# Kernel tuning notes

Hardware: AMD Instinct MI355X
Metric: run time of the kernel (lower is better)

Reference implementation:

```python
import jax, jax.numpy as jnp
import numpy as np


def setup_inputs() -> dict:
    key = jax.random.key(0)
    k1, k2 = jax.random.split(key)
    B, H, W = 4, 512, 512
    win = 5
    x = jax.random.normal(k1, (B, 3, H, W), dtype=jnp.float32)
    f = jax.random.uniform(k2, (B, win * win, H, W), dtype=jnp.float32)
    return {"x": x, "f": f, "window": win}


def reference(x, f, window):
    # x: [B, 3, H, W], f: [B, window^2, H, W]
    w = window
    p = w // 2
    B, C, H, W = x.shape
    xp = jnp.pad(x, ((0, 0), (0, 0), (p, p), (p, p)))  # ZeroPad2d(w//2)
    # One-hot conv2d == extract the (i, j) shifted window for each of w*w taps.
    # patches: [B, C, w*w, H, W]; tap order matches build_window (row-major).
    patches = jnp.stack(
        [xp[:, :, i:i + H, j:j + W] for i in range(w) for j in range(w)],
        axis=2,
    )
    # Per-pixel weighted sum over the w*w taps, same filter f for each color.
    y = jnp.einsum('bckhw,bkhw->bchw', patches, f)
    return y
```

## Files before the change

kernel.cpp:

```cpp
#include <hip/hip_runtime.h>

#define Bd   4
#define Cc   3
#define Hd   512
#define Wd   512
#define WIN  5
#define PAD  2
#define PLANE (Hd * Wd)

#define TW   128
#define TH   8
#define LDS_COLS (TW + 2 * PAD)
#define LDS_ROWS (TH + 2 * PAD)

typedef float f4 __attribute__((ext_vector_type(4)));

__global__ __launch_bounds__(256, 4) void filter_layer_kernel(
    const float* __restrict__ x,
    const float* __restrict__ f,
    float* __restrict__ y)
{
    __shared__ __align__(16) float xs[Cc][LDS_ROWS][LDS_COLS];

    const int b  = blockIdx.z;
    const int h0 = blockIdx.y * TH;
    const int w0 = blockIdx.x * TW;
    const int tid = threadIdx.x;

    const int tile_n = Cc * LDS_ROWS * LDS_COLS;
    for (int idx = tid; idx < tile_n; idx += 256) {
        const int col = idx % LDS_COLS;
        const int t   = idx / LDS_COLS;
        const int row = t % LDS_ROWS;
        const int c   = t / LDS_ROWS;
        const int gh  = h0 + row - PAD;
        const int gw  = w0 + col - PAD;
        float v = 0.0f;
        if (gh >= 0 && gh < Hd && gw >= 0 && gw < Wd)
            v = x[(((size_t)b * Cc + c) * Hd + gh) * Wd + gw];
        xs[c][row][col] = v;
    }
    __syncthreads();

    const int tx   = tid & 31;
    const int ty   = tid >> 5;
    const int wloc = tx * 4;
    const int h    = h0 + ty;
    const int gw   = w0 + wloc;

    const float* fb = f + ((size_t)b * (WIN * WIN)) * PLANE
                        + (size_t)h * Wd + gw;

    float acc[Cc][4];
    #pragma unroll
    for (int c = 0; c < Cc; ++c)
        #pragma unroll
        for (int p = 0; p < 4; ++p) acc[c][p] = 0.0f;

    f4 fcur[WIN], fnxt[WIN];
    #pragma unroll
    for (int j = 0; j < WIN; ++j)
        fcur[j] = __builtin_nontemporal_load(
            (const f4*)(fb + (size_t)j * PLANE));

    #pragma unroll 1
    for (int i = 0; i < WIN; ++i) {
        if (i + 1 < WIN) {
            const float* fr = fb + (size_t)(i + 1) * WIN * PLANE;
            #pragma unroll
            for (int j = 0; j < WIN; ++j)
                fnxt[j] = __builtin_nontemporal_load(
                    (const f4*)(fr + (size_t)j * PLANE));
        }

        float xr[Cc][8];
        #pragma unroll
        for (int c = 0; c < Cc; ++c) {
            const f4* src = (const f4*)&xs[c][ty + i][wloc];
            const f4 a  = src[0];
            const f4 b4 = src[1];
            xr[c][0] = a.x;  xr[c][1] = a.y;  xr[c][2] = a.z;  xr[c][3] = a.w;
            xr[c][4] = b4.x; xr[c][5] = b4.y; xr[c][6] = b4.z; xr[c][7] = b4.w;
        }

        #pragma unroll
        for (int j = 0; j < WIN; ++j) {
            const f4 fv = fcur[j];
            #pragma unroll
            for (int c = 0; c < Cc; ++c) {
                acc[c][0] += fv.x * xr[c][j + 0];
                acc[c][1] += fv.y * xr[c][j + 1];
                acc[c][2] += fv.z * xr[c][j + 2];
                acc[c][3] += fv.w * xr[c][j + 3];
            }
        }

        #pragma unroll
        for (int j = 0; j < WIN; ++j) fcur[j] = fnxt[j];
    }

    #pragma unroll
    for (int c = 0; c < Cc; ++c) {
        f4 o;
        o.x = acc[c][0]; o.y = acc[c][1]; o.z = acc[c][2]; o.w = acc[c][3];
        *(f4*)(y + (((size_t)b * Cc + c) * Hd + h) * Wd + gw) = o;
    }
}

extern "C" void kernel_launch(void* const* d_in, const int* in_sizes, int n_in,
                              void* d_out, int out_size, void* d_ws, size_t ws_size,
                              hipStream_t stream) {
    const float* x = (const float*)d_in[0];
    const float* f = (const float*)d_in[1];
    float* y = (float*)d_out;

    dim3 grid(Wd / TW, Hd / TH, Bd);
    filter_layer_kernel<<<grid, dim3(256), 0, stream>>>(x, f, y);
}
```

Measured before the change: 167.0 us.

## Use full-width row tiles with 8 pixels per thread and vectorized halo load

Each block now covers four full 512-wide rows instead of a 128x8 tile, so the horizontal halo disappears and the LDS fill becomes coalesced float4 loads with only the edge pads zeroed. Each thread computes 8 pixels instead of 4, doubling the filter loads in flight and the register usage, with launch bounds lowered to 2 blocks per SIMD. Nontemporal loads of the filter are replaced with ordinary loads. The intent is to cut the scalar index math and halo overhead and raise memory-level parallelism on this streaming, bandwidth-bound kernel, at the cost of fewer blocks (512) and lower occupancy.

```diff
diff --git a/kernel.cpp b/kernel.cpp
--- a/kernel.cpp
+++ b/kernel.cpp
@@ -1,109 +1,116 @@
 #include <hip/hip_runtime.h>
 
-#define Bd   4
-#define Cc   3
-#define Hd   512
-#define Wd   512
-#define WIN  5
-#define PAD  2
+#define Bd    4
+#define Cc    3
+#define Hd    512
+#define Wd    512
+#define WIN   5
 #define PLANE (Hd * Wd)
 
-#define TW   128
-#define TH   8
-#define LDS_COLS (TW + 2 * PAD)
-#define LDS_ROWS (TH + 2 * PAD)
+#define TH    4
+#define LROWS (TH + 4)
+#define LROW  520
 
 typedef float f4 __attribute__((ext_vector_type(4)));
 
-__global__ __launch_bounds__(256, 4) void filter_layer_kernel(
+__global__ __launch_bounds__(256, 2) void filter_layer_kernel(
     const float* __restrict__ x,
     const float* __restrict__ f,
     float* __restrict__ y)
 {
-    __shared__ __align__(16) float xs[Cc][LDS_ROWS][LDS_COLS];
+    __shared__ __align__(16) float xs[Cc][LROWS][LROW];
 
-    const int b  = blockIdx.z;
-    const int h0 = blockIdx.y * TH;
-    const int w0 = blockIdx.x * TW;
+    const int b   = blockIdx.y;
+    const int h0  = blockIdx.x * TH;
     const int tid = threadIdx.x;
 
-    const int tile_n = Cc * LDS_ROWS * LDS_COLS;
-    for (int idx = tid; idx < tile_n; idx += 256) {
-        const int col = idx % LDS_COLS;
-        const int t   = idx / LDS_COLS;
-        const int row = t % LDS_ROWS;
-        const int c   = t / LDS_ROWS;
-        const int gh  = h0 + row - PAD;
-        const int gw  = w0 + col - PAD;
-        float v = 0.0f;
-        if (gh >= 0 && gh < Hd && gw >= 0 && gw < Wd)
-            v = x[(((size_t)b * Cc + c) * Hd + gh) * Wd + gw];
-        xs[c][row][col] = v;
+    {
+        const int lane32 = tid & 31;
+        const int rowi   = tid >> 5;
+        const int gh     = h0 + rowi - 2;
+        const bool hok   = (gh >= 0) && (gh < Hd);
+        #pragma unroll
+        for (int c = 0; c < Cc; ++c) {
+            const float* xrow = x + (((size_t)b * Cc + c) * Hd + gh) * Wd;
+            #pragma unroll
+            for (int g = 0; g < 4; ++g) {
+                const int gw = (g * 32 + lane32) * 4;
+                f4 v = {0.f, 0.f, 0.f, 0.f};
+                if (hok) v = *(const f4*)(xrow + gw);
+                *(f4*)&xs[c][rowi][gw + 4] = v;
+            }
+            if (lane32 == 0) {
+                xs[c][rowi][2]   = 0.f; xs[c][rowi][3]   = 0.f;
+                xs[c][rowi][516] = 0.f; xs[c][rowi][517] = 0.f;
+            }
+        }
     }
     __syncthreads();
 
-    const int tx   = tid & 31;
-    const int ty   = tid >> 5;
-    const int wloc = tx * 4;
-    const int h    = h0 + ty;
-    const int gw   = w0 + wloc;
+    const int lane = tid & 63;
+    const int rw   = tid >> 6;
+    const int h    = h0 + rw;
+    const int px0  = lane * 8;
 
-    const float* fb = f + ((size_t)b * (WIN * WIN)) * PLANE
-                        + (size_t)h * Wd + gw;
+    const float* fb = f + ((size_t)b * WIN * WIN) * PLANE
+                        + (size_t)h * Wd + px0;
 
-    float acc[Cc][4];
+    float acc[Cc][8];
     #pragma unroll
     for (int c = 0; c < Cc; ++c)
         #pragma unroll
-        for (int p = 0; p < 4; ++p) acc[c][p] = 0.0f;
+        for (int p = 0; p < 8; ++p) acc[c][p] = 0.f;
 
-    f4 fcur[WIN], fnxt[WIN];
+    f4 fc[2 * WIN], fn[2 * WIN];
     #pragma unroll
-    for (int j = 0; j < WIN; ++j)
-        fcur[j] = __builtin_nontemporal_load(
-            (const f4*)(fb + (size_t)j * PLANE));
+    for (int j = 0; j < WIN; ++j) {
+        fc[2 * j]     = *(const f4*)(fb + (size_t)j * PLANE);
+        fc[2 * j + 1] = *(const f4*)(fb + (size_t)j * PLANE + 4);
+    }
 
     #pragma unroll 1
     for (int i = 0; i < WIN; ++i) {
         if (i + 1 < WIN) {
             const float* fr = fb + (size_t)(i + 1) * WIN * PLANE;
             #pragma unroll
-            for (int j = 0; j < WIN; ++j)
-                fnxt[j] = __builtin_nontemporal_load(
-                    (const f4*)(fr + (size_t)j * PLANE));
+            for (int j = 0; j < WIN; ++j) {
+                fn[2 * j]     = *(const f4*)(fr + (size_t)j * PLANE);
+                fn[2 * j + 1] = *(const f4*)(fr + (size_t)j * PLANE + 4);
+            }
         }
 
-        float xr[Cc][8];
+        float xr[Cc][16];
         #pragma unroll
-        for (int c = 0; c < Cc; ++c) {
-            const f4* src = (const f4*)&xs[c][ty + i][wloc];
-            const f4 a  = src[0];
-            const f4 b4 = src[1];
-            xr[c][0] = a.x;  xr[c][1] = a.y;  xr[c][2] = a.z;  xr[c][3] = a.w;
-            xr[c][4] = b4.x; xr[c][5] = b4.y; xr[c][6] = b4.z; xr[c][7] = b4.w;
-        }
+        for (int c = 0; c < Cc; ++c)
+            #pragma unroll
+            for (int g = 0; g < 4; ++g)
+                *(f4*)&xr[c][g * 4] = *(const f4*)&xs[c][rw + i][px0 + g * 4];
 
         #pragma unroll
         for (int j = 0; j < WIN; ++j) {
-            const f4 fv = fcur[j];
             #pragma unroll
             for (int c = 0; c < Cc; ++c) {
-                acc[c][0] += fv.x * xr[c][j + 0];
-                acc[c][1] += fv.y * xr[c][j + 1];
-                acc[c][2] += fv.z * xr[c][j + 2];
-                acc[c][3] += fv.w * xr[c][j + 3];
+                #pragma unroll
+                for (int p = 0; p < 8; ++p) {
+                    const float fv = (p < 4)
+                        ? ((const float*)&fc[2 * j])[p]
+                        : ((const float*)&fc[2 * j + 1])[p - 4];
+                    acc[c][p] += fv * xr[c][p + j + 2];
+                }
             }
         }
 
         #pragma unroll
-        for (int j = 0; j < WIN; ++j) fcur[j] = fnxt[j];
+        for (int t = 0; t < 2 * WIN; ++t) fc[t] = fn[t];
     }
 
     #pragma unroll
     for (int c = 0; c < Cc; ++c) {
-        f4 o;
-        o.x = acc[c][0]; o.y = acc[c][1]; o.z = acc[c][2]; o.w = acc[c][3];
-        *(f4*)(y + (((size_t)b * Cc + c) * Hd + h) * Wd + gw) = o;
+        float* yp = y + (((size_t)b * Cc + c) * Hd + h) * Wd + px0;
+        f4 o0 = {acc[c][0], acc[c][1], acc[c][2], acc[c][3]};
+        f4 o1 = {acc[c][4], acc[c][5], acc[c][6], acc[c][7]};
+        *(f4*)yp       = o0;
+        *(f4*)(yp + 4) = o1;
     }
 }
 
@@ -114,6 +121,6 @@
     const float* f = (const float*)d_in[1];
     float* y = (float*)d_out;
 
-    dim3 grid(Wd / TW, Hd / TH, Bd);
+    dim3 grid(Hd / TH, Bd);
     filter_layer_kernel<<<grid, dim3(256), 0, stream>>>(x, f, y);
 }
```

Result: no change. 168.5 us (+0.9%).

## Drop LDS staging; read x halo directly from global per row

Applied to the files above, without the earlier changes.

Removes the shared-memory tile and barrier. Each 128-thread block now handles one full image row and loads neighbouring x vectors straight from global memory (L1/L2 cached), with boundary guards. Output is written with nontemporal stores. This trades the LDS fill and sync for redundant global x reads across rows and threads, relying on caches to absorb them, while the dominant f stream stays the same.

```diff
diff --git a/kernel.cpp b/kernel.cpp
--- a/kernel.cpp
+++ b/kernel.cpp
@@ -1,67 +1,35 @@
 #include <hip/hip_runtime.h>
 
-#define Bd   4
-#define Cc   3
-#define Hd   512
-#define Wd   512
-#define WIN  5
-#define PAD  2
+#define Bd    4
+#define Cc    3
+#define Hd    512
+#define Wd    512
+#define WIN   5
 #define PLANE (Hd * Wd)
-
-#define TW   128
-#define TH   8
-#define LDS_COLS (TW + 2 * PAD)
-#define LDS_ROWS (TH + 2 * PAD)
 
 typedef float f4 __attribute__((ext_vector_type(4)));
 
-__global__ __launch_bounds__(256, 4) void filter_layer_kernel(
+__global__ __launch_bounds__(128, 4) void filter_layer_kernel(
     const float* __restrict__ x,
     const float* __restrict__ f,
     float* __restrict__ y)
 {
-    __shared__ __align__(16) float xs[Cc][LDS_ROWS][LDS_COLS];
-
-    const int b  = blockIdx.z;
-    const int h0 = blockIdx.y * TH;
-    const int w0 = blockIdx.x * TW;
-    const int tid = threadIdx.x;
-
-    const int tile_n = Cc * LDS_ROWS * LDS_COLS;
-    for (int idx = tid; idx < tile_n; idx += 256) {
-        const int col = idx % LDS_COLS;
-        const int t   = idx / LDS_COLS;
-        const int row = t % LDS_ROWS;
-        const int c   = t / LDS_ROWS;
-        const int gh  = h0 + row - PAD;
-        const int gw  = w0 + col - PAD;
-        float v = 0.0f;
-        if (gh >= 0 && gh < Hd && gw >= 0 && gw < Wd)
-            v = x[(((size_t)b * Cc + c) * Hd + gh) * Wd + gw];
-        xs[c][row][col] = v;
-    }
-    __syncthreads();
-
-    const int tx   = tid & 31;
-    const int ty   = tid >> 5;
-    const int wloc = tx * 4;
-    const int h    = h0 + ty;
-    const int gw   = w0 + wloc;
+    const int h   = blockIdx.x;
+    const int b   = blockIdx.y;
+    const int px0 = (int)threadIdx.x * 4;
 
     const float* fb = f + ((size_t)b * (WIN * WIN)) * PLANE
-                        + (size_t)h * Wd + gw;
+                        + (size_t)h * Wd + px0;
 
-    float acc[Cc][4];
-    #pragma unroll
-    for (int c = 0; c < Cc; ++c)
-        #pragma unroll
-        for (int p = 0; p < 4; ++p) acc[c][p] = 0.0f;
+    float acc[Cc][4] = {};
 
-    f4 fcur[WIN], fnxt[WIN];
+    const bool g0 = (px0 >= 4);
+    const bool g2 = (px0 <= Wd - 8);
+
+    f4 fc[WIN], fn[WIN];
     #pragma unroll
     for (int j = 0; j < WIN; ++j)
-        fcur[j] = __builtin_nontemporal_load(
-            (const f4*)(fb + (size_t)j * PLANE));
+        fc[j] = __builtin_nontemporal_load((const f4*)(fb + (size_t)j * PLANE));
 
     #pragma unroll 1
     for (int i = 0; i < WIN; ++i) {
@@ -69,41 +37,46 @@
             const float* fr = fb + (size_t)(i + 1) * WIN * PLANE;
             #pragma unroll
             for (int j = 0; j < WIN; ++j)
-                fnxt[j] = __builtin_nontemporal_load(
+                fn[j] = __builtin_nontemporal_load(
                     (const f4*)(fr + (size_t)j * PLANE));
         }
 
-        float xr[Cc][8];
+        const int  gh  = h + i - 2;
+        const bool rok = (gh >= 0) && (gh < Hd);
+
         #pragma unroll
         for (int c = 0; c < Cc; ++c) {
-            const f4* src = (const f4*)&xs[c][ty + i][wloc];
-            const f4 a  = src[0];
-            const f4 b4 = src[1];
-            xr[c][0] = a.x;  xr[c][1] = a.y;  xr[c][2] = a.z;  xr[c][3] = a.w;
-            xr[c][4] = b4.x; xr[c][5] = b4.y; xr[c][6] = b4.z; xr[c][7] = b4.w;
-        }
+            const float* xp = x + ((size_t)b * Cc + c) * PLANE
+                                + (size_t)gh * Wd + px0;
+            f4 x0 = {0.f, 0.f, 0.f, 0.f};
+            f4 x1 = {0.f, 0.f, 0.f, 0.f};
+            f4 x2 = {0.f, 0.f, 0.f, 0.f};
+            if (rok) {
+                x1 = *(const f4*)(xp);
+                if (g0) x0 = *(const f4*)(xp - 4);
+                if (g2) x2 = *(const f4*)(xp + 4);
+            }
+            float xr[12];
+            *(f4*)&xr[0] = x0; *(f4*)&xr[4] = x1; *(f4*)&xr[8] = x2;
 
-        #pragma unroll
-        for (int j = 0; j < WIN; ++j) {
-            const f4 fv = fcur[j];
             #pragma unroll
-            for (int c = 0; c < Cc; ++c) {
-                acc[c][0] += fv.x * xr[c][j + 0];
-                acc[c][1] += fv.y * xr[c][j + 1];
-                acc[c][2] += fv.z * xr[c][j + 2];
-                acc[c][3] += fv.w * xr[c][j + 3];
+            for (int j = 0; j < WIN; ++j) {
+                acc[c][0] += fc[j].x * xr[j + 2];
+                acc[c][1] += fc[j].y * xr[j + 3];
+                acc[c][2] += fc[j].z * xr[j + 4];
+                acc[c][3] += fc[j].w * xr[j + 5];
             }
         }
 
         #pragma unroll
-        for (int j = 0; j < WIN; ++j) fcur[j] = fnxt[j];
+        for (int j = 0; j < WIN; ++j) fc[j] = fn[j];
     }
 
     #pragma unroll
     for (int c = 0; c < Cc; ++c) {
-        f4 o;
-        o.x = acc[c][0]; o.y = acc[c][1]; o.z = acc[c][2]; o.w = acc[c][3];
-        *(f4*)(y + (((size_t)b * Cc + c) * Hd + h) * Wd + gw) = o;
+        f4 o = {acc[c][0], acc[c][1], acc[c][2], acc[c][3]};
+        __builtin_nontemporal_store(
+            o, (f4*)(y + (((size_t)b * Cc + c) * Hd + h) * Wd + px0));
     }
 }
 
@@ -114,6 +87,6 @@
     const float* f = (const float*)d_in[1];
     float* y = (float*)d_out;
 
-    dim3 grid(Wd / TW, Hd / TH, Bd);
-    filter_layer_kernel<<<grid, dim3(256), 0, stream>>>(x, f, y);
+    dim3 grid(Hd, Bd);
+    filter_layer_kernel<<<grid, dim3(128), 0, stream>>>(x, f, y);
 }
```

After: 165.9 us. No clear change (-0.7%).
